# Performance work log

Hardware: AMD Instinct MI355X
Metric: run time of the kernel (lower is better)

Reference implementation:

```python
import jax, jax.numpy as jnp
import numpy as np

N_ITER = 3  # GenSP(n_iter=3)


def _gen_sp(x, stoken):
    """Faithful JAX port of ssn_iter + visualize_spixels (GenSP.forward).

    Instead of materializing the dense (B,S,P) affinity via sparse_coo->to_dense,
    we keep the exact 9-candidate structure: each pixel has 9 candidate
    superpixels (its init superpixel and 8 grid neighbors). The bmm-based
    centroid update is mathematically identical to a masked segment-sum over
    those candidates, and the dense argmax over S equals the argmax over the 9
    candidates (all other columns are exactly 0).
    """
    B, C, H, W = x.shape
    sh = sw = stoken
    nsh, nsw = H // sh, W // sw
    S = nsh * nsw          # number of superpixels
    P = H * W              # number of pixels

    xs = jax.lax.stop_gradient(x)  # torch runs all SSN iterations under no_grad

    # adaptive_avg_pool2d with exact divisibility == block mean
    cent = xs.reshape(B, C, nsh, sh, nsw, sw).mean(axis=(3, 5)).reshape(B, C, S)  # (B,C,S)

    # nearest-neighbor upsampled init label map (B-independent)
    lab = jnp.arange(S, dtype=jnp.int32).reshape(nsh, nsw)
    lab = jnp.repeat(jnp.repeat(lab, sh, axis=0), sw, axis=1).reshape(P)  # (P,)
    lx, ly = lab % nsw, lab // nsw

    offs = [(dy, dx) for dy in (-1, 0, 1) for dx in (-1, 0, 1)]  # matches r-nsw, r, r+nsw ordering
    cand = jnp.stack([lab + dy * nsw + dx for dy, dx in offs])   # (9,P) candidate spixel ids
    valid = jnp.stack([(lx + dx >= 0) & (lx + dx < nsw) &
                       (ly + dy >= 0) & (ly + dy < nsh) for dy, dx in offs])  # (9,P)
    cand_safe = jnp.where(valid, cand, 0)

    px = xs.reshape(B, C, P).transpose(0, 2, 1)  # (B,P,C)

    def affinity(cent_b, px_b):
        # PairwiseDistFunction: squared L2 pixel->candidate centroid, inf if invalid
        ct = cent_b.T  # (S,C)
        d = jnp.stack([jnp.sum((px_b - ct[cand_safe[k]]) ** 2, axis=-1)
                       for k in range(9)])             # (9,P)
        logits = jnp.where(valid, -d, -jnp.inf)
        return jnp.where(valid, jax.nn.softmax(logits, axis=0), 0.0)  # (9,P)

    def centroid_update(aff, px_b):
        # == bmm(abs_affinity, px) / abs_affinity.sum(2), via segment sums
        num = jnp.zeros((S, C), px_b.dtype)
        den = jnp.zeros((S,), px_b.dtype)
        for k in range(9):
            num = num + jax.ops.segment_sum(aff[k][:, None] * px_b, cand_safe[k], num_segments=S)
            den = den + jax.ops.segment_sum(aff[k], cand_safe[k], num_segments=S)
        return (num / (den[:, None] + 1e-16)).T  # (C,S)

    def hard_labels(cent_b, px_b):
        c = cent_b
        for _ in range(N_ITER - 1):
            c = centroid_update(affinity(c, px_b), px_b)
        aff = affinity(c, px_b)                         # final abs_affinity (sparse form)
        best = jnp.argmax(aff, axis=0)                  # (P,)
        return jnp.take_along_axis(cand_safe, best[None], axis=0)[0]

    labels = jax.vmap(hard_labels)(cent, px)[0]         # torch paints only image[0]

    # visualize_spixels: per-superpixel per-channel mean, painted back
    px0 = x[0].reshape(C, P).T                          # (P,C), grads flow here
    sums = jax.ops.segment_sum(px0, labels, num_segments=S)
    cnt = jax.ops.segment_sum(jnp.ones((P,), px0.dtype), labels, num_segments=S)
    means = sums / jnp.maximum(cnt, 1.0)[:, None]       # (S,C)
    return means[labels].T.reshape(1, C, H, W)


def setup_inputs() -> dict:
    key = jax.random.key(0)
    x = jax.random.normal(key, (1, 64, 384, 384), dtype=jnp.float32)
    return {"x": x, "stoken": 16}


def reference(x, stoken):
    return _gen_sp(x, stoken)
```

## Files before the change

kernel.cpp:

```cpp
#include <hip/hip_runtime.h>
#include <math.h>


#define NC   64
#define IMW  384
#define HWP  (384*384)
#define NSH  24
#define NSW  24
#define NS   (NSH*NSW)
#define NCP  (NS*4)
#define NBG  (NS*8)

__global__ __launch_bounds__(256) void k_cent_part(const float* __restrict__ x,
                                                   double* __restrict__ centp) {
    int bg = blockIdx.x, b = bg >> 2, g = bg & 3;
    int by = b / NSW, bx = b % NSW;
    int t = threadIdx.x, q = t >> 2, r = t & 3;
    const float* gp = x + (size_t)q * HWP + (size_t)(by * 16 + g * 4) * IMW + bx * 16 + r * 4;
    double s = 0.0;
    #pragma unroll
    for (int j = 0; j < 4; ++j) {
        float4 v = *(const float4*)(gp + (size_t)j * IMW);
        s += (double)v.x; s += (double)v.y; s += (double)v.z; s += (double)v.w;
    }
    s += __shfl_xor(s, 1, 64);
    s += __shfl_xor(s, 2, 64);
    if (r == 0) centp[(size_t)bg * NC + q] = s;
}

__global__ __launch_bounds__(64) void k_cent_red(const double* __restrict__ centp,
                                                 double* __restrict__ cent,
                                                 double* __restrict__ cnorm) {
    int s = blockIdx.x, c = threadIdx.x;
    double v = centp[(size_t)(s * 4 + 0) * NC + c] + centp[(size_t)(s * 4 + 1) * NC + c]
             + centp[(size_t)(s * 4 + 2) * NC + c] + centp[(size_t)(s * 4 + 3) * NC + c];
    v *= (1.0 / 256.0);
    cent[s * NC + c] = v;
    double n2 = v * v;
    #pragma unroll
    for (int off = 32; off >= 1; off >>= 1) n2 += __shfl_down(n2, off, 64);
    if (c == 0) cnorm[s] = n2;
}

__global__ __launch_bounds__(64) void k_iter(const float* __restrict__ x,
        const double* __restrict__ cent, const double* __restrict__ cnorm,
        double* __restrict__ bnum, double* __restrict__ bden) {
    int bg = blockIdx.x, b = bg >> 3, g = bg & 7;
    int by = b / NSW, bx = b % NSW;
    int t = threadIdx.x;
    int p = t & 31, h = t >> 5;
    __shared__ double scent[9][64];
    __shared__ double aff[9][33];

    int cand[9]; bool vld[9];
    #pragma unroll
    for (int k = 0; k < 9; ++k) {
        int cy = by + k / 3 - 1, cx = bx + k % 3 - 1;
        vld[k] = (cy >= 0) && (cy < NSH) && (cx >= 0) && (cx < NSW);
        cand[k] = vld[k] ? (cy * NSW + cx) : 0;
    }

    #pragma unroll
    for (int j = 0; j < 9; ++j)
        scent[j][t] = cent[(size_t)cand[j] * NC + t];
    __syncthreads();

    const float* xp = x + (size_t)(by * 16 + g * 2 + (p >> 4)) * IMW + bx * 16 + (p & 15);
    double dot[9] = {0, 0, 0, 0, 0, 0, 0, 0, 0};
    #pragma unroll 4
    for (int i = 0; i < 32; ++i) {
        int c = h * 32 + i;
        double xv = (double)xp[(size_t)c * HWP];
        #pragma unroll
        for (int k = 0; k < 9; ++k)
            dot[k] = fma(xv, scent[k][c], dot[k]);
    }
    #pragma unroll
    for (int k = 0; k < 9; ++k) dot[k] += __shfl_xor(dot[k], 32, 64);

    double d[9], m = -1e300;
    #pragma unroll
    for (int k = 0; k < 9; ++k) {
        d[k] = fma(dot[k], -2.0, cnorm[cand[k]]);
        if (vld[k]) m = fmax(m, -d[k]);
    }
    double e[9], ss = 0.0;
    #pragma unroll
    for (int k = 0; k < 9; ++k) { e[k] = vld[k] ? exp(-d[k] - m) : 0.0; ss += e[k]; }
    double inv = 1.0 / ss;
    #pragma unroll
    for (int k = 0; k < 9; ++k) {
        e[k] *= inv;
        if (h == 0) aff[k][p] = e[k];
    }

    #pragma unroll
    for (int k = 0; k < 9; ++k) {
        double dn = e[k];
        #pragma unroll
        for (int off = 16; off >= 1; off >>= 1) dn += __shfl_down(dn, off, 64);
        if (t == 0) bden[(size_t)bg * 9 + k] = dn;
    }
    __syncthreads();

    int c = t;
    double acc[9] = {0, 0, 0, 0, 0, 0, 0, 0, 0};
    const float* xq = x + (size_t)c * HWP + (size_t)(by * 16 + g * 2) * IMW + bx * 16;
    #pragma unroll
    for (int r = 0; r < 2; ++r) {
        #pragma unroll
        for (int q = 0; q < 4; ++q) {
            float4 xw = *(const float4*)(xq + (size_t)r * IMW + q * 4);
            int pp = r * 16 + q * 4;
            #pragma unroll
            for (int k = 0; k < 9; ++k) {
                acc[k] = fma(aff[k][pp + 0], (double)xw.x, acc[k]);
                acc[k] = fma(aff[k][pp + 1], (double)xw.y, acc[k]);
                acc[k] = fma(aff[k][pp + 2], (double)xw.z, acc[k]);
                acc[k] = fma(aff[k][pp + 3], (double)xw.w, acc[k]);
            }
        }
    }
    #pragma unroll
    for (int k = 0; k < 9; ++k) bnum[((size_t)bg * 9 + k) * NC + c] = acc[k];
}

__global__ __launch_bounds__(64) void k_gather_cent(const double* __restrict__ bnum,
                                                    const double* __restrict__ bden,
                                                    double* __restrict__ cent,
                                                    double* __restrict__ cnorm) {
    int s = blockIdx.x, c = threadIdx.x;
    int sy = s / NSW, sx = s % NSW;
    double num = 0.0, den = 0.0;
    #pragma unroll
    for (int k = 0; k < 9; ++k) {
        int by2 = sy - (k / 3 - 1), bx2 = sx - (k % 3 - 1);
        if (by2 >= 0 && by2 < NSH && bx2 >= 0 && bx2 < NSW) {
            int b2 = by2 * NSW + bx2;
            #pragma unroll
            for (int g = 0; g < 8; ++g) {
                int bg = b2 * 8 + g;
                num += bnum[((size_t)bg * 9 + k) * NC + c];
                den += bden[(size_t)bg * 9 + k];
            }
        }
    }
    double v = num / (den + 1e-16);
    cent[s * NC + c] = v;
    double n2 = v * v;
    #pragma unroll
    for (int off = 32; off >= 1; off >>= 1) n2 += __shfl_down(n2, off, 64);
    if (c == 0) cnorm[s] = n2;
}

__global__ __launch_bounds__(64) void k_final(const float* __restrict__ x,
        const double* __restrict__ cent, const double* __restrict__ cnorm,
        int* __restrict__ labels,
        double* __restrict__ bnum, double* __restrict__ bden) {
    int bg = blockIdx.x, b = bg >> 3, g = bg & 7;
    int by = b / NSW, bx = b % NSW;
    int t = threadIdx.x;
    int p = t & 31, h = t >> 5;
    __shared__ double scent[9][64];
    __shared__ double aff[9][33];

    int cand[9]; bool vld[9];
    #pragma unroll
    for (int k = 0; k < 9; ++k) {
        int cy = by + k / 3 - 1, cx = bx + k % 3 - 1;
        vld[k] = (cy >= 0) && (cy < NSH) && (cx >= 0) && (cx < NSW);
        cand[k] = vld[k] ? (cy * NSW + cx) : 0;
    }

    #pragma unroll
    for (int j = 0; j < 9; ++j)
        scent[j][t] = cent[(size_t)cand[j] * NC + t];
    __syncthreads();

    const float* xp = x + (size_t)(by * 16 + g * 2 + (p >> 4)) * IMW + bx * 16 + (p & 15);
    double dot[9] = {0, 0, 0, 0, 0, 0, 0, 0, 0};
    #pragma unroll 4
    for (int i = 0; i < 32; ++i) {
        int c = h * 32 + i;
        double xv = (double)xp[(size_t)c * HWP];
        #pragma unroll
        for (int k = 0; k < 9; ++k)
            dot[k] = fma(xv, scent[k][c], dot[k]);
    }
    #pragma unroll
    for (int k = 0; k < 9; ++k) dot[k] += __shfl_xor(dot[k], 32, 64);

    double bestd = 1e300; int bk = 0;
    #pragma unroll
    for (int k = 0; k < 9; ++k) {
        double dv = fma(dot[k], -2.0, cnorm[cand[k]]);
        if (vld[k] && dv < bestd) { bestd = dv; bk = k; }
    }
    if (h == 0) {
        labels[(size_t)(by * 16 + g * 2 + (p >> 4)) * IMW + bx * 16 + (p & 15)] =
            (by + bk / 3 - 1) * NSW + (bx + bk % 3 - 1);
        #pragma unroll
        for (int k = 0; k < 9; ++k) aff[k][p] = (bk == k) ? 1.0 : 0.0;
    }

    #pragma unroll
    for (int k = 0; k < 9; ++k) {
        int cnt = (bk == k);
        #pragma unroll
        for (int off = 16; off >= 1; off >>= 1) cnt += __shfl_down(cnt, off, 64);
        if (t == 0) bden[(size_t)bg * 9 + k] = (double)cnt;
    }
    __syncthreads();

    int c = t;
    double acc[9] = {0, 0, 0, 0, 0, 0, 0, 0, 0};
    const float* xq = x + (size_t)c * HWP + (size_t)(by * 16 + g * 2) * IMW + bx * 16;
    #pragma unroll
    for (int r = 0; r < 2; ++r) {
        #pragma unroll
        for (int q = 0; q < 4; ++q) {
            float4 xw = *(const float4*)(xq + (size_t)r * IMW + q * 4);
            int pp = r * 16 + q * 4;
            #pragma unroll
            for (int k = 0; k < 9; ++k) {
                acc[k] = fma(aff[k][pp + 0], (double)xw.x, acc[k]);
                acc[k] = fma(aff[k][pp + 1], (double)xw.y, acc[k]);
                acc[k] = fma(aff[k][pp + 2], (double)xw.z, acc[k]);
                acc[k] = fma(aff[k][pp + 3], (double)xw.w, acc[k]);
            }
        }
    }
    #pragma unroll
    for (int k = 0; k < 9; ++k) bnum[((size_t)bg * 9 + k) * NC + c] = acc[k];
}

__global__ __launch_bounds__(64) void k_means_(const double* __restrict__ bnum,
                                               const double* __restrict__ bden,
                                               float* __restrict__ means) {
    int s = blockIdx.x, c = threadIdx.x;
    int sy = s / NSW, sx = s % NSW;
    double num = 0.0, den = 0.0;
    #pragma unroll
    for (int k = 0; k < 9; ++k) {
        int by2 = sy - (k / 3 - 1), bx2 = sx - (k % 3 - 1);
        if (by2 >= 0 && by2 < NSH && bx2 >= 0 && bx2 < NSW) {
            int b2 = by2 * NSW + bx2;
            #pragma unroll
            for (int g = 0; g < 8; ++g) {
                int bg = b2 * 8 + g;
                num += bnum[((size_t)bg * 9 + k) * NC + c];
                den += bden[(size_t)bg * 9 + k];
            }
        }
    }
    means[s * NC + c] = (float)(num / fmax(den, 1.0));
}

__global__ __launch_bounds__(256) void k_paint(const int* __restrict__ labels,
                                               const float* __restrict__ means,
                                               float* __restrict__ out) {
    int p0 = (blockIdx.x * 256 + threadIdx.x) * 4;
    int4 lb = *(const int4*)&labels[p0];
    int c0 = blockIdx.y * 4;
    #pragma unroll
    for (int j = 0; j < 4; ++j) {
        int c = c0 + j;
        float4 o;
        o.x = means[lb.x * NC + c];
        o.y = means[lb.y * NC + c];
        o.z = means[lb.z * NC + c];
        o.w = means[lb.w * NC + c];
        *(float4*)&out[(size_t)c * HWP + p0] = o;
    }
}

extern "C" void kernel_launch(void* const* d_in, const int* in_sizes, int n_in,
                              void* d_out, int out_size, void* d_ws, size_t ws_size,
                              hipStream_t stream) {
    const float* x = (const float*)d_in[0];
    float* out = (float*)d_out;
    char* ws = (char*)d_ws;
    char* od = (char*)d_out;

    constexpr size_t CENTP_B = (size_t)NCP * NC * 8;
    constexpr size_t CENT_B  = (size_t)NS * NC * 8;
    constexpr size_t CNRM_B  = (size_t)NS * 8;
    constexpr size_t BNUM_B  = (size_t)NBG * 9 * NC * 8;
    constexpr size_t BDEN_B  = (size_t)NBG * 9 * 8;
    constexpr size_t LAB_B   = (size_t)HWP * 4;
    constexpr size_t MEANS_B = (size_t)NS * NC * 4;
    constexpr size_t T_PAINT = LAB_B + MEANS_B;
    constexpr size_t T_CENT  = T_PAINT + 2 * (CENT_B + CNRM_B);
    constexpr size_t T_ALL   = T_CENT + CENTP_B + BNUM_B + BDEN_B;

    int* labels = (int*)ws;
    float* means = (float*)(ws + LAB_B);
    double *centA, *centB, *cnormA, *cnormB, *centp, *bnum, *bden;
    if (ws_size >= T_ALL) {
        centA  = (double*)(ws + T_PAINT);
        centB  = (double*)(ws + T_PAINT + CENT_B);
        cnormA = (double*)(ws + T_PAINT + 2 * CENT_B);
        cnormB = (double*)(ws + T_PAINT + 2 * CENT_B + CNRM_B);
        centp  = (double*)(ws + T_CENT);
        bnum   = (double*)(ws + T_CENT + CENTP_B);
        bden   = (double*)(ws + T_CENT + CENTP_B + BNUM_B);
    } else if (ws_size >= T_CENT) {
        centA  = (double*)(ws + T_PAINT);
        centB  = (double*)(ws + T_PAINT + CENT_B);
        cnormA = (double*)(ws + T_PAINT + 2 * CENT_B);
        cnormB = (double*)(ws + T_PAINT + 2 * CENT_B + CNRM_B);
        centp  = (double*)od;
        bnum   = (double*)(od + CENTP_B);
        bden   = (double*)(od + CENTP_B + BNUM_B);
    } else {
        centp  = (double*)od;
        bnum   = (double*)(od + CENTP_B);
        bden   = (double*)(od + CENTP_B + BNUM_B);
        centA  = (double*)(od + CENTP_B + BNUM_B + BDEN_B);
        centB  = (double*)(od + CENTP_B + BNUM_B + BDEN_B + CENT_B);
        cnormA = (double*)(od + CENTP_B + BNUM_B + BDEN_B + 2 * CENT_B);
        cnormB = (double*)(od + CENTP_B + BNUM_B + BDEN_B + 2 * CENT_B + CNRM_B);
    }

    k_cent_part<<<NCP, 256, 0, stream>>>(x, centp);
    k_cent_red<<<NS, 64, 0, stream>>>(centp, centA, cnormA);
    k_iter<<<NBG, 64, 0, stream>>>(x, centA, cnormA, bnum, bden);
    k_gather_cent<<<NS, 64, 0, stream>>>(bnum, bden, centB, cnormB);
    k_iter<<<NBG, 64, 0, stream>>>(x, centB, cnormB, bnum, bden);
    k_gather_cent<<<NS, 64, 0, stream>>>(bnum, bden, centA, cnormA);
    k_final<<<NBG, 64, 0, stream>>>(x, centA, cnormA, labels, bnum, bden);
    k_means_<<<NS, 64, 0, stream>>>(bnum, bden, means);
    k_paint<<<dim3(HWP / 1024, NC / 4), 256, 0, stream>>>(labels, means, out);
}
```

Baseline: 122.4 us.

## Fuse centroid init kernels and software-pipeline x loads in iteration kernels

Merges the two-kernel initial centroid computation (partial sums plus reduction) into one kernel per superpixel, removing a launch and the intermediate buffer. In k_iter and k_final, the channel loads for the distance dot product are double-buffered in register batches of eight and issued before the barrier. The float4 loads for the centroid numerator are also hoisted ahead of the softmax, so memory latency overlaps with compute. Holding more values in registers raises register pressure and may lower occupancy.

```diff
diff --git a/kernel.cpp b/kernel.cpp
--- a/kernel.cpp
+++ b/kernel.cpp
@@ -8,39 +8,43 @@
 #define NSH  24
 #define NSW  24
 #define NS   (NSH*NSW)
-#define NCP  (NS*4)
 #define NBG  (NS*8)
 
-__global__ __launch_bounds__(256) void k_cent_part(const float* __restrict__ x,
-                                                   double* __restrict__ centp) {
-    int bg = blockIdx.x, b = bg >> 2, g = bg & 3;
-    int by = b / NSW, bx = b % NSW;
+__global__ __launch_bounds__(256) void k_cent_init(const float* __restrict__ x,
+                                                   double* __restrict__ cent,
+                                                   double* __restrict__ cnorm) {
+    int s = blockIdx.x, by = s / NSW, bx = s % NSW;
     int t = threadIdx.x, q = t >> 2, r = t & 3;
-    const float* gp = x + (size_t)q * HWP + (size_t)(by * 16 + g * 4) * IMW + bx * 16 + r * 4;
-    double s = 0.0;
-    #pragma unroll
-    for (int j = 0; j < 4; ++j) {
-        float4 v = *(const float4*)(gp + (size_t)j * IMW);
-        s += (double)v.x; s += (double)v.y; s += (double)v.z; s += (double)v.w;
-    }
-    s += __shfl_xor(s, 1, 64);
-    s += __shfl_xor(s, 2, 64);
-    if (r == 0) centp[(size_t)bg * NC + q] = s;
-}
-
-__global__ __launch_bounds__(64) void k_cent_red(const double* __restrict__ centp,
-                                                 double* __restrict__ cent,
-                                                 double* __restrict__ cnorm) {
-    int s = blockIdx.x, c = threadIdx.x;
-    double v = centp[(size_t)(s * 4 + 0) * NC + c] + centp[(size_t)(s * 4 + 1) * NC + c]
-             + centp[(size_t)(s * 4 + 2) * NC + c] + centp[(size_t)(s * 4 + 3) * NC + c];
-    v *= (1.0 / 256.0);
-    cent[s * NC + c] = v;
-    double n2 = v * v;
-    #pragma unroll
-    for (int off = 32; off >= 1; off >>= 1) n2 += __shfl_down(n2, off, 64);
-    if (c == 0) cnorm[s] = n2;
-}
+    __shared__ double wl[4];
+    const float* gp = x + (size_t)q * HWP + (size_t)(by * 16) * IMW + bx * 16 + r * 4;
+    double sg[4];
+    #pragma unroll
+    for (int g = 0; g < 4; ++g) {
+        double s2 = 0.0;
+        #pragma unroll
+        for (int j = 0; j < 4; ++j) {
+            float4 v = *(const float4*)(gp + (size_t)(g * 4 + j) * IMW);
+            s2 += (double)v.x; s2 += (double)v.y; s2 += (double)v.z; s2 += (double)v.w;
+        }
+        s2 += __shfl_xor(s2, 1, 64);
+        s2 += __shfl_xor(s2, 2, 64);
+        sg[g] = s2;
+    }
+    double v = (((sg[0] + sg[1]) + sg[2]) + sg[3]) * (1.0 / 256.0);
+    if (r == 0) cent[s * NC + q] = v;
+    double n2 = (r == 0) ? v * v : 0.0;
+    #pragma unroll
+    for (int off = 32; off >= 1; off >>= 1) n2 += __shfl_xor(n2, off, 64);
+    if ((t & 63) == 0) wl[t >> 6] = n2;
+    __syncthreads();
+    if (t == 0) cnorm[s] = ((wl[0] + wl[1]) + wl[2]) + wl[3];
+}
+
+#define LOAD8(buf, base) { _Pragma("unroll") \
+    for (int j = 0; j < 8; ++j) buf[j] = xp[(size_t)(h * 32 + (base) + j) * HWP]; }
+#define FMA8(buf, base) { _Pragma("unroll") \
+    for (int j = 0; j < 8; ++j) { double xv_ = (double)buf[j]; _Pragma("unroll") \
+        for (int k = 0; k < 9; ++k) dot[k] = fma(xv_, scent[k][h * 32 + (base) + j], dot[k]); } }
 
 __global__ __launch_bounds__(64) void k_iter(const float* __restrict__ x,
         const double* __restrict__ cent, const double* __restrict__ cnorm,
@@ -59,24 +63,30 @@
         vld[k] = (cy >= 0) && (cy < NSH) && (cx >= 0) && (cx < NSW);
         cand[k] = vld[k] ? (cy * NSW + cx) : 0;
     }
-
     #pragma unroll
     for (int j = 0; j < 9; ++j)
         scent[j][t] = cent[(size_t)cand[j] * NC + t];
-    __syncthreads();
 
     const float* xp = x + (size_t)(by * 16 + g * 2 + (p >> 4)) * IMW + bx * 16 + (p & 15);
     double dot[9] = {0, 0, 0, 0, 0, 0, 0, 0, 0};
-    #pragma unroll 4
-    for (int i = 0; i < 32; ++i) {
-        int c = h * 32 + i;
-        double xv = (double)xp[(size_t)c * HWP];
-        #pragma unroll
-        for (int k = 0; k < 9; ++k)
-            dot[k] = fma(xv, scent[k][c], dot[k]);
-    }
+    float b0[8], b1[8];
+    LOAD8(b0, 0);
+    __syncthreads();
+    LOAD8(b1, 8);   FMA8(b0, 0);
+    LOAD8(b0, 16);  FMA8(b1, 8);
+    LOAD8(b1, 24);  FMA8(b0, 16);
+    FMA8(b1, 24);
     #pragma unroll
     for (int k = 0; k < 9; ++k) dot[k] += __shfl_xor(dot[k], 32, 64);
+
+    int c = t;
+    const float* xq = x + (size_t)c * HWP + (size_t)(by * 16 + g * 2) * IMW + bx * 16;
+    float4 fq[8];
+    #pragma unroll
+    for (int r = 0; r < 2; ++r)
+        #pragma unroll
+        for (int qq = 0; qq < 4; ++qq)
+            fq[r * 4 + qq] = *(const float4*)(xq + (size_t)r * IMW + qq * 4);
 
     double d[9], m = -1e300;
     #pragma unroll
@@ -93,7 +103,6 @@
         e[k] *= inv;
         if (h == 0) aff[k][p] = e[k];
     }
-
     #pragma unroll
     for (int k = 0; k < 9; ++k) {
         double dn = e[k];
@@ -103,15 +112,13 @@
     }
     __syncthreads();
 
-    int c = t;
     double acc[9] = {0, 0, 0, 0, 0, 0, 0, 0, 0};
-    const float* xq = x + (size_t)c * HWP + (size_t)(by * 16 + g * 2) * IMW + bx * 16;
     #pragma unroll
     for (int r = 0; r < 2; ++r) {
         #pragma unroll
-        for (int q = 0; q < 4; ++q) {
-            float4 xw = *(const float4*)(xq + (size_t)r * IMW + q * 4);
-            int pp = r * 16 + q * 4;
+        for (int qq = 0; qq < 4; ++qq) {
+            float4 xw = fq[r * 4 + qq];
+            int pp = r * 16 + qq * 4;
             #pragma unroll
             for (int k = 0; k < 9; ++k) {
                 acc[k] = fma(aff[k][pp + 0], (double)xw.x, acc[k]);
@@ -171,24 +178,30 @@
         vld[k] = (cy >= 0) && (cy < NSH) && (cx >= 0) && (cx < NSW);
         cand[k] = vld[k] ? (cy * NSW + cx) : 0;
     }
-
     #pragma unroll
     for (int j = 0; j < 9; ++j)
         scent[j][t] = cent[(size_t)cand[j] * NC + t];
-    __syncthreads();
 
     const float* xp = x + (size_t)(by * 16 + g * 2 + (p >> 4)) * IMW + bx * 16 + (p & 15);
     double dot[9] = {0, 0, 0, 0, 0, 0, 0, 0, 0};
-    #pragma unroll 4
-    for (int i = 0; i < 32; ++i) {
-        int c = h * 32 + i;
-        double xv = (double)xp[(size_t)c * HWP];
-        #pragma unroll
-        for (int k = 0; k < 9; ++k)
-            dot[k] = fma(xv, scent[k][c], dot[k]);
-    }
+    float b0[8], b1[8];
+    LOAD8(b0, 0);
+    __syncthreads();
+    LOAD8(b1, 8);   FMA8(b0, 0);
+    LOAD8(b0, 16);  FMA8(b1, 8);
+    LOAD8(b1, 24);  FMA8(b0, 16);
+    FMA8(b1, 24);
     #pragma unroll
     for (int k = 0; k < 9; ++k) dot[k] += __shfl_xor(dot[k], 32, 64);
+
+    int c = t;
+    const float* xq = x + (size_t)c * HWP + (size_t)(by * 16 + g * 2) * IMW + bx * 16;
+    float4 fq[8];
+    #pragma unroll
+    for (int r = 0; r < 2; ++r)
+        #pragma unroll
+        for (int qq = 0; qq < 4; ++qq)
+            fq[r * 4 + qq] = *(const float4*)(xq + (size_t)r * IMW + qq * 4);
 
     double bestd = 1e300; int bk = 0;
     #pragma unroll
@@ -202,7 +215,6 @@
         #pragma unroll
         for (int k = 0; k < 9; ++k) aff[k][p] = (bk == k) ? 1.0 : 0.0;
     }
-
     #pragma unroll
     for (int k = 0; k < 9; ++k) {
         int cnt = (bk == k);
@@ -212,15 +224,13 @@
     }
     __syncthreads();
 
-    int c = t;
     double acc[9] = {0, 0, 0, 0, 0, 0, 0, 0, 0};
-    const float* xq = x + (size_t)c * HWP + (size_t)(by * 16 + g * 2) * IMW + bx * 16;
     #pragma unroll
     for (int r = 0; r < 2; ++r) {
         #pragma unroll
-        for (int q = 0; q < 4; ++q) {
-            float4 xw = *(const float4*)(xq + (size_t)r * IMW + q * 4);
-            int pp = r * 16 + q * 4;
+        for (int qq = 0; qq < 4; ++qq) {
+            float4 xw = fq[r * 4 + qq];
+            int pp = r * 16 + qq * 4;
             #pragma unroll
             for (int k = 0; k < 9; ++k) {
                 acc[k] = fma(aff[k][pp + 0], (double)xw.x, acc[k]);
@@ -282,7 +292,6 @@
     char* ws = (char*)d_ws;
     char* od = (char*)d_out;
 
-    constexpr size_t CENTP_B = (size_t)NCP * NC * 8;
     constexpr size_t CENT_B  = (size_t)NS * NC * 8;
     constexpr size_t CNRM_B  = (size_t)NS * 8;
     constexpr size_t BNUM_B  = (size_t)NBG * 9 * NC * 8;
@@ -291,39 +300,35 @@
     constexpr size_t MEANS_B = (size_t)NS * NC * 4;
     constexpr size_t T_PAINT = LAB_B + MEANS_B;
     constexpr size_t T_CENT  = T_PAINT + 2 * (CENT_B + CNRM_B);
-    constexpr size_t T_ALL   = T_CENT + CENTP_B + BNUM_B + BDEN_B;
+    constexpr size_t T_ALL   = T_CENT + BNUM_B + BDEN_B;
 
     int* labels = (int*)ws;
     float* means = (float*)(ws + LAB_B);
-    double *centA, *centB, *cnormA, *cnormB, *centp, *bnum, *bden;
+    double *centA, *centB, *cnormA, *cnormB, *bnum, *bden;
     if (ws_size >= T_ALL) {
         centA  = (double*)(ws + T_PAINT);
         centB  = (double*)(ws + T_PAINT + CENT_B);
         cnormA = (double*)(ws + T_PAINT + 2 * CENT_B);
         cnormB = (double*)(ws + T_PAINT + 2 * CENT_B + CNRM_B);
-        centp  = (double*)(ws + T_CENT);
-        bnum   = (double*)(ws + T_CENT + CENTP_B);
-        bden   = (double*)(ws + T_CENT + CENTP_B + BNUM_B);
+        bnum   = (double*)(ws + T_CENT);
+        bden   = (double*)(ws + T_CENT + BNUM_B);
     } else if (ws_size >= T_CENT) {
         centA  = (double*)(ws + T_PAINT);
         centB  = (double*)(ws + T_PAINT + CENT_B);
         cnormA = (double*)(ws + T_PAINT + 2 * CENT_B);
         cnormB = (double*)(ws + T_PAINT + 2 * CENT_B + CNRM_B);
-        centp  = (double*)od;
-        bnum   = (double*)(od + CENTP_B);
-        bden   = (double*)(od + CENTP_B + BNUM_B);
+        bnum   = (double*)od;
+        bden   = (double*)(od + BNUM_B);
     } else {
-        centp  = (double*)od;
-        bnum   = (double*)(od + CENTP_B);
-        bden   = (double*)(od + CENTP_B + BNUM_B);
-        centA  = (double*)(od + CENTP_B + BNUM_B + BDEN_B);
-        centB  = (double*)(od + CENTP_B + BNUM_B + BDEN_B + CENT_B);
-        cnormA = (double*)(od + CENTP_B + BNUM_B + BDEN_B + 2 * CENT_B);
-        cnormB = (double*)(od + CENTP_B + BNUM_B + BDEN_B + 2 * CENT_B + CNRM_B);
-    }
-
-    k_cent_part<<<NCP, 256, 0, stream>>>(x, centp);
-    k_cent_red<<<NS, 64, 0, stream>>>(centp, centA, cnormA);
+        bnum   = (double*)od;
+        bden   = (double*)(od + BNUM_B);
+        centA  = (double*)(od + BNUM_B + BDEN_B);
+        centB  = (double*)(od + BNUM_B + BDEN_B + CENT_B);
+        cnormA = (double*)(od + BNUM_B + BDEN_B + 2 * CENT_B);
+        cnormB = (double*)(od + BNUM_B + BDEN_B + 2 * CENT_B + CNRM_B);
+    }
+
+    k_cent_init<<<NS, 256, 0, stream>>>(x, centA, cnormA);
     k_iter<<<NBG, 64, 0, stream>>>(x, centA, cnormA, bnum, bden);
     k_gather_cent<<<NS, 64, 0, stream>>>(bnum, bden, centB, cnormB);
     k_iter<<<NBG, 64, 0, stream>>>(x, centB, cnormB, bnum, bden);
```

After: 124.7 us. No clear change (+1.9%).
